# Kernel tuning notes

Measured on AMD Instinct MI355X. Metric: run time of the kernel, lower is better.

## Reference

```python
import jax, jax.numpy as jnp
import numpy as np

B, S, D, H = 4, 2048, 1024, 16
HD = D // H  # head_dim = 64


def setup_inputs() -> dict:
    key = jax.random.key(0)
    ks = jax.random.split(key, 4)
    scale = 0.02
    return {
        "x": jax.random.normal(ks[0], (B, S, D), dtype=jnp.float32),
        "W_attn": jax.random.normal(ks[1], (D, 3 * D), dtype=jnp.float32) * scale,
        "b_attn": jnp.zeros((3 * D,), dtype=jnp.float32),
        "W_proj": jax.random.normal(ks[2], (D, D), dtype=jnp.float32) * scale,
        "b_proj": jnp.zeros((D,), dtype=jnp.float32),
    }


def reference(x, W_attn, b_attn, W_proj, b_proj):
    b, s, d = x.shape
    qkv = x @ W_attn + b_attn                      # [b, s, 3d]
    q, k, v = jnp.split(qkv, 3, axis=2)
    # [b, s, d] -> [b, h, s, hd]
    def to_heads(t):
        return t.reshape(b, s, H, HD).transpose(0, 2, 1, 3)
    q, k, v = to_heads(q), to_heads(k), to_heads(v)
    scores = jnp.einsum("bhqd,bhkd->bhqk", q, k) / jnp.sqrt(jnp.float32(HD))
    causal = jnp.tril(jnp.ones((s, s), dtype=bool))  # [s, s]
    scores = jnp.where(causal[None, None], scores, jnp.float32(-jnp.inf))
    probs = jax.nn.softmax(scores, axis=-1)
    y = jnp.einsum("bhqk,bhkd->bhqd", probs, v)    # [b, h, s, hd]
    y = y.transpose(0, 2, 1, 3).reshape(b, s, d)
    return y @ W_proj + b_proj
```

## Files before the change

kernel.cpp:

```cpp
#include <hip/hip_runtime.h>
#include <hip/hip_bf16.h>
#include <type_traits>

#define SQ    2048
#define DIM   1024
#define NH    16
#define HDIM  64
#define BATCH 4

typedef unsigned short u16;
typedef __bf16 bf16x8 __attribute__((ext_vector_type(8)));
typedef float  f32x4  __attribute__((ext_vector_type(4)));
typedef u16    u16x8  __attribute__((ext_vector_type(8)));

#define QSCALE 0.180336880f

__device__ __forceinline__ u16 f2bf(float f) {
  union { float f; unsigned u; } v; v.f = f;
  unsigned r = v.u + 0x7fffu + ((v.u >> 16) & 1u);
  return (u16)(r >> 16);
}

__device__ __forceinline__ void gll16(const u16* g, u16* l) {
  __builtin_amdgcn_global_load_lds((const __attribute__((address_space(1))) void*)g,
                                   (__attribute__((address_space(3))) void*)l,
                                   16, 0, 0);
}

__global__ __launch_bounds__(256)
void f32_to_bf16_vec(const float* __restrict__ in, u16* __restrict__ out, int n4)
{
  const int i = blockIdx.x * blockDim.x + threadIdx.x;
  if (i < n4) {
    const float4 v = ((const float4*)in)[i];
    ushort4 o;
    o.x = f2bf(v.x); o.y = f2bf(v.y); o.z = f2bf(v.z); o.w = f2bf(v.w);
    ((ushort4*)out)[i] = o;
  }
}

__global__ void transpose_f32_bf16(const float* __restrict__ in, u16* __restrict__ out,
                                   int R, int C)
{
  __shared__ u16 tile[32][33];
  const int bx = blockIdx.x * 32, by = blockIdx.y * 32;
  const int tx = threadIdx.x, ty = threadIdx.y;
  #pragma unroll
  for (int i = 0; i < 32; i += 8)
    tile[ty + i][tx] = f2bf(in[(size_t)(by + ty + i) * C + bx + tx]);
  __syncthreads();
  #pragma unroll
  for (int i = 0; i < 32; i += 8)
    out[(size_t)(bx + ty + i) * R + by + tx] = tile[tx][ty + i];
}

template<int MODE>
__global__ __launch_bounds__(256)
void gemm_bt(const u16* __restrict__ A, const u16* __restrict__ Bt,
             const float* __restrict__ bias, int K,
             u16* __restrict__ o0, u16* __restrict__ o1, float* __restrict__ of)
{
  __shared__ __align__(16) u16 A0[128 * 32], A1[128 * 32];
  __shared__ __align__(16) u16 B0[128 * 32], B1[128 * 32];

  const int t    = threadIdx.x;
  const int lane = t & 63, wave = t >> 6;
  const int l15  = lane & 15, quad = lane >> 4;
  const int wm   = (wave & 1) * 64, wn = (wave >> 1) * 64;
  const int m0   = blockIdx.y * 128, n0 = blockIdx.x * 128;

  const int srow = wave * 32 + (lane >> 2);
  const int scol = (lane & 3) * 8;

  f32x4 acc[4][4] = {};

  for (int k0 = 0; k0 < K; k0 += 64) {
    const u16* ga = A  + (size_t)(m0 + srow) * K + k0 + scol;
    const u16* gb = Bt + (size_t)(n0 + srow) * K + k0 + scol;
    gll16(ga,              &A0[(wave * 32)      * 32]);
    gll16(ga + 32,         &A1[(wave * 32)      * 32]);
    gll16(ga + 16 * K,     &A0[(wave * 32 + 16) * 32]);
    gll16(ga + 16 * K + 32,&A1[(wave * 32 + 16) * 32]);
    gll16(gb,              &B0[(wave * 32)      * 32]);
    gll16(gb + 32,         &B1[(wave * 32)      * 32]);
    gll16(gb + 16 * K,     &B0[(wave * 32 + 16) * 32]);
    gll16(gb + 16 * K + 32,&B1[(wave * 32 + 16) * 32]);
    __syncthreads();

    #pragma unroll
    for (int ks = 0; ks < 2; ++ks) {
      const u16* Als = ks ? A1 : A0;
      const u16* Bls = ks ? B1 : B0;
      bf16x8 af[4], bfr[4];
      #pragma unroll
      for (int i = 0; i < 4; ++i) af[i]  = *(const bf16x8*)&Als[(wm + 16*i + l15) * 32 + quad * 8];
      #pragma unroll
      for (int j = 0; j < 4; ++j) bfr[j] = *(const bf16x8*)&Bls[(wn + 16*j + l15) * 32 + quad * 8];
      #pragma unroll
      for (int i = 0; i < 4; ++i)
        #pragma unroll
        for (int j = 0; j < 4; ++j)
          acc[i][j] = (MODE == 2)
            ? __builtin_amdgcn_mfma_f32_16x16x32_bf16(bfr[j], af[i], acc[i][j], 0, 0, 0)
            : __builtin_amdgcn_mfma_f32_16x16x32_bf16(af[i], bfr[j], acc[i][j], 0, 0, 0);
    }
    __syncthreads();
  }

  if (MODE == 2) {
    #pragma unroll
    for (int j = 0; j < 4; ++j) {
      #pragma unroll
      for (int r = 0; r < 4; ++r) {
        const int d = n0 + wn + 16*j + quad * 4 + r;
        const float bn = bias[d];
        const int h = d >> 6, hd = d & 63;
        #pragma unroll
        for (int i = 0; i < 4; ++i) {
          const int m = m0 + wm + 16*i + l15;
          const int b = m >> 11, s = m & 2047;
          o0[(((size_t)(b * NH + h)) * HDIM + hd) * SQ + s] = f2bf(acc[i][j][r] + bn);
        }
      }
    }
  } else {
    #pragma unroll
    for (int j = 0; j < 4; ++j) {
      const int n = n0 + wn + 16*j + l15;
      const float bn = bias[n];
      #pragma unroll
      for (int i = 0; i < 4; ++i) {
        #pragma unroll
        for (int r = 0; r < 4; ++r) {
          const int m = m0 + wm + 16*i + quad * 4 + r;
          const float val = acc[i][j][r] + bn;
          if (MODE == 1) {
            const int sec = n >> 10, d = n & 1023;
            const int h = d >> 6, hd = d & 63;
            const int b = m >> 11, s = m & 2047;
            const int bh = b * NH + h;
            if (sec == 0) o0[((size_t)bh * SQ + s) * HDIM + hd] = f2bf(val * QSCALE);
            else          o1[((size_t)bh * SQ + s) * HDIM + hd] = f2bf(val);
          } else {
            of[(size_t)m * DIM + n] = val;
          }
        }
      }
    }
  }
}

#define LP 72

__global__ __launch_bounds__(256)
void attn_fused(const u16* __restrict__ q_ws, const u16* __restrict__ k_ws,
                const u16* __restrict__ v_t, u16* __restrict__ y_ws)
{
  __shared__ __align__(16) u16 Kls[2][2][64 * 32];
  __shared__ __align__(16) u16 Vls[2][2][64 * 32];
  __shared__ __align__(16) u16 Pls[4][32 * LP];

  const int bh = blockIdx.x;
  const int pair = blockIdx.y;
  const int b = bh >> 4, h = bh & 15;
  const int t = threadIdx.x;
  const int lane = t & 63, wave = t >> 6;
  const int l15 = lane & 15, quad = lane >> 4;

  const u16* Q  = q_ws + (size_t)bh * SQ * HDIM;
  const u16* Kp = k_ws + (size_t)bh * SQ * HDIM;
  const u16* Vp = v_t  + (size_t)bh * HDIM * SQ;

  const int sr = wave * 16 + (lane >> 2);
  const int sc = (lane & 3) * 8;

  auto stage = [&](int kv0, int buf) {
    gll16(&Kp[(size_t)(kv0 + sr) * HDIM + sc],      &Kls[buf][0][wave * 512]);
    gll16(&Kp[(size_t)(kv0 + sr) * HDIM + sc + 32], &Kls[buf][1][wave * 512]);
    gll16(&Vp[(size_t)sr * SQ + kv0 + sc],          &Vls[buf][0][wave * 512]);
    gll16(&Vp[(size_t)sr * SQ + kv0 + sc + 32],     &Vls[buf][1][wave * 512]);
  };

  auto run_phase = [&](int qt) {
    const int qrow = qt * 128 + wave * 32;

    bf16x8 qf[2][2];
    #pragma unroll
    for (int qi = 0; qi < 2; ++qi)
      #pragma unroll
      for (int ks = 0; ks < 2; ++ks)
        qf[qi][ks] = *(const bf16x8*)&Q[(size_t)(qrow + 16*qi + l15) * HDIM + ks * 32 + quad * 8];

    f32x4 o[2][4] = {};
    float l_q[2] = {};

    const int last = 2 * qt + (wave >> 1);
    const int ntiles = 2 * qt + 2;

    auto compute = [&](int kv0, int buf, auto maskc) {
      constexpr bool MASKED = decltype(maskc)::value;
      f32x4 st[4][2] = {};
      #pragma unroll
      for (int ks = 0; ks < 2; ++ks) {
        const u16* Kh = Kls[buf][ks];
        #pragma unroll
        for (int kt = 0; kt < 4; ++kt) {
          bf16x8 kf = *(const bf16x8*)&Kh[(16*kt + l15) * 32 + quad * 8];
          #pragma unroll
          for (int qi = 0; qi < 2; ++qi)
            st[kt][qi] = __builtin_amdgcn_mfma_f32_16x16x32_bf16(kf, qf[qi][ks], st[kt][qi], 0, 0, 0);
        }
      }

      #pragma unroll
      for (int qi = 0; qi < 2; ++qi) {
        const int q = qrow + 16*qi + l15;
        float rsum = 0.f;
        #pragma unroll
        for (int kt = 0; kt < 4; ++kt)
          #pragma unroll
          for (int r = 0; r < 4; ++r) {
            float pv = exp2f(st[kt][qi][r]);
            if (MASKED && (kv0 + 16*kt + quad*4 + r) > q) pv = 0.f;
            st[kt][qi][r] = pv;
            rsum += pv;
          }
        l_q[qi] += rsum;
      }

      #pragma unroll
      for (int qi = 0; qi < 2; ++qi)
        #pragma unroll
        for (int kt = 0; kt < 4; ++kt) {
          union { __hip_bfloat162 h2[2]; ushort4 u4; } pk;
          pk.h2[0] = __float22bfloat162_rn(make_float2(st[kt][qi][0], st[kt][qi][1]));
          pk.h2[1] = __float22bfloat162_rn(make_float2(st[kt][qi][2], st[kt][qi][3]));
          *(ushort4*)&Pls[wave][(16*qi + l15) * LP + 16*kt + quad * 4] = pk.u4;
        }

      #pragma unroll
      for (int ks = 0; ks < 2; ++ks) {
        const u16* Vh = Vls[buf][ks];
        bf16x8 vf[4];
        #pragma unroll
        for (int n = 0; n < 4; ++n)
          vf[n] = *(const bf16x8*)&Vh[(16*n + l15) * 32 + quad * 8];
        #pragma unroll
        for (int mi = 0; mi < 2; ++mi) {
          bf16x8 pa = *(const bf16x8*)&Pls[wave][(16*mi + l15) * LP + ks * 32 + quad * 8];
          #pragma unroll
          for (int n = 0; n < 4; ++n)
            o[mi][n] = __builtin_amdgcn_mfma_f32_16x16x32_bf16(pa, vf[n], o[mi][n], 0, 0, 0);
        }
      }
    };

    stage(0, 0);
    for (int kvt = 0; kvt < ntiles; ++kvt) {
      const int cur = kvt & 1;
      __syncthreads();
      if (kvt + 1 < ntiles) stage((kvt + 1) * 64, cur ^ 1);
      if (kvt <= last) {
        if (kvt < last) compute(kvt * 64, cur, std::integral_constant<bool,false>{});
        else            compute(kvt * 64, cur, std::integral_constant<bool,true>{});
      }
    }
    __syncthreads();

    #pragma unroll
    for (int qi = 0; qi < 2; ++qi) {
      l_q[qi] += __shfl_xor(l_q[qi], 16);
      l_q[qi] += __shfl_xor(l_q[qi], 32);
    }
    #pragma unroll
    for (int mi = 0; mi < 2; ++mi)
      #pragma unroll
      for (int r = 0; r < 4; ++r) {
        const float lr = __shfl(l_q[mi], quad * 4 + r);
        const float inv = 1.0f / lr;
        const int qg = qrow + 16*mi + quad * 4 + r;
        #pragma unroll
        for (int n = 0; n < 4; ++n)
          y_ws[((size_t)b * SQ + qg) * DIM + h * HDIM + 16*n + l15] = f2bf(o[mi][n][r] * inv);
      }
  };

  run_phase(15 - pair);
  run_phase(pair);
}

extern "C" void kernel_launch(void* const* d_in, const int* in_sizes, int n_in,
                              void* d_out, int out_size, void* d_ws, size_t ws_size,
                              hipStream_t stream)
{
  const float* x      = (const float*)d_in[0];
  const float* W_attn = (const float*)d_in[1];
  const float* b_attn = (const float*)d_in[2];
  const float* W_proj = (const float*)d_in[3];
  const float* b_proj = (const float*)d_in[4];
  float* out = (float*)d_out;

  char* ws = (char*)d_ws;
  u16* WattnT = (u16*)(ws);
  u16* WprojT = (u16*)(ws + 6291456);
  u16* xb     = (u16*)(ws + 8388608);
  u16* y_ws   = xb;
  u16* q_ws   = (u16*)(ws + 25165824);
  u16* k_ws   = (u16*)(ws + 41943040);
  u16* v_tw   = (u16*)(ws + 58720256);

  const dim3 tb(32, 8);
  transpose_f32_bf16<<<dim3(3 * DIM / 32, DIM / 32), tb, 0, stream>>>(W_attn, WattnT, DIM, 3 * DIM);
  transpose_f32_bf16<<<dim3(DIM / 32, DIM / 32), tb, 0, stream>>>(W_proj, WprojT, DIM, DIM);
  f32_to_bf16_vec<<<(BATCH * SQ * DIM / 4 + 255) / 256, 256, 0, stream>>>(x, xb, BATCH * SQ * DIM / 4);

  gemm_bt<1><<<dim3(2 * DIM / 128, BATCH * SQ / 128), 256, 0, stream>>>(
      xb, WattnT, b_attn, DIM, q_ws, k_ws, nullptr);
  gemm_bt<2><<<dim3(DIM / 128, BATCH * SQ / 128), 256, 0, stream>>>(
      xb, WattnT + (size_t)2048 * DIM, b_attn + 2048, DIM, v_tw, nullptr, nullptr);

  attn_fused<<<dim3(BATCH * NH, 8), 256, 0, stream>>>(q_ws, k_ws, v_tw, y_ws);

  gemm_bt<0><<<dim3(DIM / 128, BATCH * SQ / 128), 256, 0, stream>>>(
      y_ws, WprojT, b_proj, DIM, nullptr, nullptr, out);
}
```

Measured before the change: 284.9 us.

## Process both paired query tiles in one KV sweep to share K/V loads

New measurement: 287.5 us. About the same (+0.9%).

```diff
diff --git a/kernel.cpp b/kernel.cpp
--- a/kernel.cpp
+++ b/kernel.cpp
@@ -161,7 +161,7 @@
   __shared__ __align__(16) u16 Pls[4][32 * LP];
 
   const int bh = blockIdx.x;
-  const int pair = blockIdx.y;
+  const int p  = blockIdx.y;
   const int b = bh >> 4, h = bh & 15;
   const int t = threadIdx.x;
   const int lane = t & 63, wave = t >> 6;
@@ -170,6 +170,22 @@
   const u16* Q  = q_ws + (size_t)bh * SQ * HDIM;
   const u16* Kp = k_ws + (size_t)bh * SQ * HDIM;
   const u16* Vp = v_t  + (size_t)bh * HDIM * SQ;
+
+  const int qtH = 15 - p, qtL = p;
+  const int qrowH = qtH * 128 + wave * 32;
+  const int qrowL = qtL * 128 + wave * 32;
+
+  bf16x8 qf[4][2];
+  #pragma unroll
+  for (int qi = 0; qi < 2; ++qi)
+    #pragma unroll
+    for (int ks = 0; ks < 2; ++ks) {
+      qf[qi][ks]     = *(const bf16x8*)&Q[(size_t)(qrowH + 16*qi + l15) * HDIM + ks * 32 + quad * 8];
+      qf[2 + qi][ks] = *(const bf16x8*)&Q[(size_t)(qrowL + 16*qi + l15) * HDIM + ks * 32 + quad * 8];
+    }
+
+  f32x4 o[4][4] = {};
+  float l_q[4] = {};
 
   const int sr = wave * 16 + (lane >> 2);
   const int sc = (lane & 3) * 8;
@@ -181,112 +197,101 @@
     gll16(&Vp[(size_t)sr * SQ + kv0 + sc + 32],     &Vls[buf][1][wave * 512]);
   };
 
-  auto run_phase = [&](int qt) {
-    const int qrow = qt * 128 + wave * 32;
-
-    bf16x8 qf[2][2];
+  auto compute = [&](int kv0, int buf, int base, int qrow, auto maskc) {
+    constexpr bool MASKED = decltype(maskc)::value;
+    f32x4 st[4][2] = {};
+    #pragma unroll
+    for (int ks = 0; ks < 2; ++ks) {
+      const u16* Kh = Kls[buf][ks];
+      #pragma unroll
+      for (int kt = 0; kt < 4; ++kt) {
+        bf16x8 kf = *(const bf16x8*)&Kh[(16*kt + l15) * 32 + quad * 8];
+        #pragma unroll
+        for (int qi = 0; qi < 2; ++qi)
+          st[kt][qi] = __builtin_amdgcn_mfma_f32_16x16x32_bf16(kf, qf[base + qi][ks], st[kt][qi], 0, 0, 0);
+      }
+    }
+
+    #pragma unroll
+    for (int qi = 0; qi < 2; ++qi) {
+      const int q = qrow + 16*qi + l15;
+      float rsum = 0.f;
+      #pragma unroll
+      for (int kt = 0; kt < 4; ++kt)
+        #pragma unroll
+        for (int r = 0; r < 4; ++r) {
+          float pv = exp2f(st[kt][qi][r]);
+          if (MASKED && (kv0 + 16*kt + quad*4 + r) > q) pv = 0.f;
+          st[kt][qi][r] = pv;
+          rsum += pv;
+        }
+      l_q[base + qi] += rsum;
+    }
+
     #pragma unroll
     for (int qi = 0; qi < 2; ++qi)
       #pragma unroll
-      for (int ks = 0; ks < 2; ++ks)
-        qf[qi][ks] = *(const bf16x8*)&Q[(size_t)(qrow + 16*qi + l15) * HDIM + ks * 32 + quad * 8];
-
-    f32x4 o[2][4] = {};
-    float l_q[2] = {};
-
-    const int last = 2 * qt + (wave >> 1);
-    const int ntiles = 2 * qt + 2;
-
-    auto compute = [&](int kv0, int buf, auto maskc) {
-      constexpr bool MASKED = decltype(maskc)::value;
-      f32x4 st[4][2] = {};
-      #pragma unroll
-      for (int ks = 0; ks < 2; ++ks) {
-        const u16* Kh = Kls[buf][ks];
-        #pragma unroll
-        for (int kt = 0; kt < 4; ++kt) {
-          bf16x8 kf = *(const bf16x8*)&Kh[(16*kt + l15) * 32 + quad * 8];
-          #pragma unroll
-          for (int qi = 0; qi < 2; ++qi)
-            st[kt][qi] = __builtin_amdgcn_mfma_f32_16x16x32_bf16(kf, qf[qi][ks], st[kt][qi], 0, 0, 0);
-        }
-      }
-
-      #pragma unroll
-      for (int qi = 0; qi < 2; ++qi) {
-        const int q = qrow + 16*qi + l15;
-        float rsum = 0.f;
-        #pragma unroll
-        for (int kt = 0; kt < 4; ++kt)
-          #pragma unroll
-          for (int r = 0; r < 4; ++r) {
-            float pv = exp2f(st[kt][qi][r]);
-            if (MASKED && (kv0 + 16*kt + quad*4 + r) > q) pv = 0.f;
-            st[kt][qi][r] = pv;
-            rsum += pv;
-          }
-        l_q[qi] += rsum;
-      }
-
-      #pragma unroll
-      for (int qi = 0; qi < 2; ++qi)
-        #pragma unroll
-        for (int kt = 0; kt < 4; ++kt) {
-          union { __hip_bfloat162 h2[2]; ushort4 u4; } pk;
-          pk.h2[0] = __float22bfloat162_rn(make_float2(st[kt][qi][0], st[kt][qi][1]));
-          pk.h2[1] = __float22bfloat162_rn(make_float2(st[kt][qi][2], st[kt][qi][3]));
-          *(ushort4*)&Pls[wave][(16*qi + l15) * LP + 16*kt + quad * 4] = pk.u4;
-        }
-
-      #pragma unroll
-      for (int ks = 0; ks < 2; ++ks) {
-        const u16* Vh = Vls[buf][ks];
-        bf16x8 vf[4];
+      for (int kt = 0; kt < 4; ++kt) {
+        union { __hip_bfloat162 h2[2]; ushort4 u4; } pk;
+        pk.h2[0] = __float22bfloat162_rn(make_float2(st[kt][qi][0], st[kt][qi][1]));
+        pk.h2[1] = __float22bfloat162_rn(make_float2(st[kt][qi][2], st[kt][qi][3]));
+        *(ushort4*)&Pls[wave][(16*qi + l15) * LP + 16*kt + quad * 4] = pk.u4;
+      }
+
+    #pragma unroll
+    for (int ks = 0; ks < 2; ++ks) {
+      const u16* Vh = Vls[buf][ks];
+      bf16x8 vf[4];
+      #pragma unroll
+      for (int n = 0; n < 4; ++n)
+        vf[n] = *(const bf16x8*)&Vh[(16*n + l15) * 32 + quad * 8];
+      #pragma unroll
+      for (int mi = 0; mi < 2; ++mi) {
+        bf16x8 pa = *(const bf16x8*)&Pls[wave][(16*mi + l15) * LP + ks * 32 + quad * 8];
         #pragma unroll
         for (int n = 0; n < 4; ++n)
-          vf[n] = *(const bf16x8*)&Vh[(16*n + l15) * 32 + quad * 8];
-        #pragma unroll
-        for (int mi = 0; mi < 2; ++mi) {
-          bf16x8 pa = *(const bf16x8*)&Pls[wave][(16*mi + l15) * LP + ks * 32 + quad * 8];
-          #pragma unroll
-          for (int n = 0; n < 4; ++n)
-            o[mi][n] = __builtin_amdgcn_mfma_f32_16x16x32_bf16(pa, vf[n], o[mi][n], 0, 0, 0);
-        }
-      }
-    };
-
-    stage(0, 0);
-    for (int kvt = 0; kvt < ntiles; ++kvt) {
-      const int cur = kvt & 1;
-      __syncthreads();
-      if (kvt + 1 < ntiles) stage((kvt + 1) * 64, cur ^ 1);
-      if (kvt <= last) {
-        if (kvt < last) compute(kvt * 64, cur, std::integral_constant<bool,false>{});
-        else            compute(kvt * 64, cur, std::integral_constant<bool,true>{});
-      }
-    }
+          o[base + mi][n] = __builtin_amdgcn_mfma_f32_16x16x32_bf16(pa, vf[n], o[base + mi][n], 0, 0, 0);
+      }
+    }
+  };
+
+  const int ntiles = 2 * qtH + 2;
+  const int lastH  = 2 * qtH + (wave >> 1);
+  const int lastL  = 2 * qtL + (wave >> 1);
+
+  stage(0, 0);
+  for (int kvt = 0; kvt < ntiles; ++kvt) {
+    const int cur = kvt & 1;
+    const int kv0 = kvt * 64;
     __syncthreads();
-
-    #pragma unroll
-    for (int qi = 0; qi < 2; ++qi) {
-      l_q[qi] += __shfl_xor(l_q[qi], 16);
-      l_q[qi] += __shfl_xor(l_q[qi], 32);
-    }
+    if (kvt + 1 < ntiles) stage((kvt + 1) * 64, cur ^ 1);
+    if (kvt < lastH)       compute(kv0, cur, 0, qrowH, std::integral_constant<bool,false>{});
+    else if (kvt == lastH) compute(kv0, cur, 0, qrowH, std::integral_constant<bool,true>{});
+    if (kvt < lastL)       compute(kv0, cur, 2, qrowL, std::integral_constant<bool,false>{});
+    else if (kvt == lastL) compute(kv0, cur, 2, qrowL, std::integral_constant<bool,true>{});
+  }
+
+  #pragma unroll
+  for (int s = 0; s < 4; ++s) {
+    l_q[s] += __shfl_xor(l_q[s], 16);
+    l_q[s] += __shfl_xor(l_q[s], 32);
+  }
+  #pragma unroll
+  for (int g = 0; g < 2; ++g) {
+    const int qrow = g ? qrowL : qrowH;
+    const int base = g * 2;
     #pragma unroll
     for (int mi = 0; mi < 2; ++mi)
       #pragma unroll
       for (int r = 0; r < 4; ++r) {
-        const float lr = __shfl(l_q[mi], quad * 4 + r);
+        const float lr = __shfl(l_q[base + mi], quad * 4 + r);
         const float inv = 1.0f / lr;
         const int qg = qrow + 16*mi + quad * 4 + r;
         #pragma unroll
         for (int n = 0; n < 4; ++n)
-          y_ws[((size_t)b * SQ + qg) * DIM + h * HDIM + 16*n + l15] = f2bf(o[mi][n][r] * inv);
-      }
-  };
-
-  run_phase(15 - pair);
-  run_phase(pair);
+          y_ws[((size_t)b * SQ + qg) * DIM + h * HDIM + 16*n + l15] = f2bf(o[base + mi][n][r] * inv);
+      }
+  }
 }
 
 extern "C" void kernel_launch(void* const* d_in, const int* in_sizes, int n_in,
```
